# Kernel optimization log

Hardware: AMD Instinct MI355X
Metric: run time of the kernel (lower is better)

Reference implementation:

```python
import jax, jax.numpy as jnp
import numpy as np

B, SE, HD, ED, N, T = 64, 512, 1024, 512, 10000, 20
EOS_ID = 1
NEG_BIG = -1e9    # stand-in for -MAX_VAL encoder pad mask
MASK_VAL = -1e7   # logits_mask scatter value (-10000000.0 in torch)
M = HD + ED


def setup_inputs() -> dict:
    key = jax.random.key(0)
    ks = jax.random.split(key, 16)
    s = 0.02
    enc = jax.random.normal(ks[0], (B, SE, HD), jnp.float32)
    hidden = jax.random.normal(ks[1], (1, B, HD), jnp.float32)
    cell = jax.random.normal(ks[2], (1, B, HD), jnp.float32)
    text_lengths = jax.random.randint(ks[3], (B,), SE // 2, SE + 1)
    encoder_mask = jnp.arange(SE)[None, :] < text_lengths[:, None]  # [B,SE] bool
    embedding = jax.random.normal(ks[4], (N, ED), jnp.float32) * s
    # LSTM (PyTorch gate order i,f,g,o)
    w_ih = jax.random.normal(ks[5], (4 * HD, ED), jnp.float32) * s
    w_hh = jax.random.normal(ks[6], (4 * HD, HD), jnp.float32) * s
    b_ih = jnp.zeros((4 * HD,), jnp.float32)
    b_hh = jnp.zeros((4 * HD,), jnp.float32)
    # dense_net: Hd -> He
    w_q = jax.random.normal(ks[7], (HD, HD), jnp.float32) * s
    b_q = jnp.zeros((HD,), jnp.float32)
    # SelfAttentiveSum: Linear(Ed,Ed)+ReLU+Linear(Ed,1)
    w_k = jax.random.normal(ks[8], (ED, ED), jnp.float32) * s
    b_k = jnp.zeros((ED,), jnp.float32)
    w_ko = jax.random.normal(ks[9], (ED,), jnp.float32) * s
    b_ko = jnp.zeros((), jnp.float32)
    # MLP: Linear(M,M)+ReLU+Linear(M,N)
    w_m1 = jax.random.normal(ks[10], (M, M), jnp.float32) * s
    b_m1 = jnp.zeros((M,), jnp.float32)
    w_m2 = jax.random.normal(ks[11], (N, M), jnp.float32) * s
    b_m2 = jnp.zeros((N,), jnp.float32)
    return dict(encoded_hidden_embeddings=enc, hidden=hidden, cell=cell,
                text_lengths=text_lengths, encoder_mask=encoder_mask,
                embedding=embedding, w_ih=w_ih, w_hh=w_hh, b_ih=b_ih, b_hh=b_hh,
                w_q=w_q, b_q=b_q, w_k=w_k, b_k=b_k, w_ko=w_ko, b_ko=b_ko,
                w_m1=w_m1, b_m1=b_m1, w_m2=w_m2, b_m2=b_m2)


def _decode(enc, h0, c0, encoder_mask, embedding, w_ih, w_hh, b_ih, b_hh,
            w_q, b_q, w_k, b_k, w_ko, b_ko, w_m1, b_m1, w_m2, b_m2):
    pad_mask = jnp.where(encoder_mask, 0.0, NEG_BIG).astype(enc.dtype)  # [B,SE]
    sent = enc[:, 0, :]  # [B,HD] sentence representation (dropout is identity in eval)

    def step(carry, t):
        h, c, inp, logits_mask, buf = carry
        # --- LSTM cell (single step) ---
        gates = inp @ w_ih.T + b_ih + h @ w_hh.T + b_hh  # [B,4HD]
        i, f, g, o = jnp.split(gates, 4, axis=-1)
        c = jax.nn.sigmoid(f) * c + jax.nn.sigmoid(i) * jnp.tanh(g)
        h = jax.nn.sigmoid(o) * jnp.tanh(c)
        # --- attention over encoder states ---
        q = h @ w_q.T + b_q                                   # [B,HD]
        score = jnp.einsum('bsh,bh->bs', enc, q) + pad_mask    # [B,SE]
        w = jax.nn.softmax(score, axis=1)
        attn_enc = jnp.einsum('bs,bsh->bh', w, enc)            # [B,HD]
        # --- self-attentive sum over previously predicted label embeddings ---
        valid = jnp.arange(T) < jnp.maximum(t, 1)              # step 0: zeros row 0 valid
        k = jax.nn.relu(buf @ w_k.T + b_k) @ w_ko + b_ko       # [B,T]
        k = jnp.where(valid[None, :], k, NEG_BIG)
        sw = jax.nn.softmax(k, axis=1)
        attn_last = jnp.einsum('bt,bte->be', sw, buf)          # [B,ED]
        # --- MLP ---
        m = jnp.concatenate([sent + attn_enc, inp + attn_last], axis=-1)  # [B,M]
        logits = jax.nn.relu(m @ w_m1.T + b_m1) @ w_m2.T + b_m2 + logits_mask  # [B,N]
        next_ids = jnp.argmax(logits, axis=-1)                 # [B]
        pred_emb = embedding[next_ids]                          # [B,ED]
        buf = buf.at[:, t].set(pred_emb)
        logits_mask = logits_mask.at[jnp.arange(B), next_ids].set(MASK_VAL)
        logits_mask = logits_mask.at[:, EOS_ID].set(0.0)
        return (h, c, pred_emb, logits_mask, buf), (logits, next_ids)

    init = (h0, c0,
            jnp.zeros((B, ED), enc.dtype),
            jnp.zeros((B, N), enc.dtype),
            jnp.zeros((B, T, ED), enc.dtype))
    _, (outs, ids) = jax.lax.scan(step, init, jnp.arange(T))
    return jnp.transpose(outs, (1, 0, 2)), jnp.transpose(ids, (1, 0))  # [B,T,N],[B,T]


def reference(encoded_hidden_embeddings, hidden, cell, text_lengths, encoder_mask,
              embedding, w_ih, w_hh, b_ih, b_hh, w_q, b_q, w_k, b_k, w_ko, b_ko,
              w_m1, b_m1, w_m2, b_m2):
    # De=1: [1,B,HD] -> [B,HD]
    return _decode(encoded_hidden_embeddings, hidden[0], cell[0], encoder_mask,
                   embedding, w_ih, w_hh, b_ih, b_hh, w_q, b_q, w_k, b_k,
                   w_ko, b_ko, w_m1, b_m1, w_m2, b_m2)
```

## Files before the change

### kernel.cpp

```cpp
#include <hip/hip_runtime.h>

#define B64 64
#define SE 512
#define HD 1024
#define ED 512
#define NV 10000
#define TT 20
#define MM 1536
#define MASK_VALF -10000000.0f

#define OFF_XA    0
#define OFF_XB    98304
#define OFF_CT    196608
#define OFF_QF    262144
#define OFF_FM    327680
#define OFF_FL    328704
#define OFF_FACC  329728
#define OFF_XT2   1378304
#define OFF_H1T   1476608
#define OFF_ARGV  1574912
#define OFF_ARGI  1654912
#define OFF_MASKT 1734912
#define OFF_BUF   2374912
#define OFF_BUFT  3030272
#define OFF_KVP   3685632
#define OFF_LP    3767552

__device__ __forceinline__ float sigmoidf_(float x) { return 1.f / (1.f + expf(-x)); }

__global__ __launch_bounds__(256) void k_init(const float* __restrict__ h0,
                                              const float* __restrict__ c0,
                                              float* __restrict__ ws) {
  int idx = blockIdx.x * 256 + threadIdx.x, stride = gridDim.x * 256;
  float* xa = ws + OFF_XA;
  float* cT = ws + OFF_CT;
  float* maskT = ws + OFF_MASKT;
  float* buf = ws + OFF_BUF;
  float* bufT = ws + OFF_BUFT;
  for (int i = idx; i < 512 * 64; i += stride) xa[i] = 0.f;
  for (int i = idx; i < NV * 64; i += stride) maskT[i] = 0.f;
  for (int i = idx; i < B64 * TT * ED; i += stride) { buf[i] = 0.f; bufT[i] = 0.f; }
  for (int i = idx; i < HD * 64; i += stride) {
    int u = i >> 6, b = i & 63;
    xa[512 * 64 + i] = h0[b * HD + u];
    cT[i] = c0[b * HD + u];
  }
}

__global__ __launch_bounds__(256) void k_cell(const float* __restrict__ xcur,
                                              const float* __restrict__ w_ih,
                                              const float* __restrict__ w_hh,
                                              const float* __restrict__ b_ih,
                                              const float* __restrict__ b_hh,
                                              float* __restrict__ cT,
                                              float* __restrict__ xnext) {
  __shared__ float wl[8 * 1536];
  int tid = threadIdx.x;
  int u0 = blockIdx.x * 2;
  for (int i = tid; i < 3072; i += 256) {
    int lr = i / 384, kq = i % 384;
    int k = kq * 4;
    int grow = (lr >> 1) * 1024 + u0 + (lr & 1);
    float4 v;
    if (k < 512) v = *(const float4*)&w_ih[(size_t)grow * 512 + k];
    else v = *(const float4*)&w_hh[(size_t)grow * 1024 + (k - 512)];
    *(float4*)&wl[lr * 1536 + k] = v;
  }
  __syncthreads();
  int lane = tid & 63, wid = tid >> 6;
  int kbase = wid * 384;
  const float* xp = xcur + (size_t)kbase * 64 + lane;
  float acc[8] = {0, 0, 0, 0, 0, 0, 0, 0};
#pragma unroll 2
  for (int k4 = 0; k4 < 96; ++k4) {
    float x0 = xp[(4 * k4 + 0) * 64];
    float x1 = xp[(4 * k4 + 1) * 64];
    float x2 = xp[(4 * k4 + 2) * 64];
    float x3 = xp[(4 * k4 + 3) * 64];
#pragma unroll
    for (int lr = 0; lr < 8; ++lr) {
      const float4 w4 = *(const float4*)&wl[lr * 1536 + kbase + 4 * k4];
      acc[lr] = fmaf(w4.x, x0, acc[lr]);
      acc[lr] = fmaf(w4.y, x1, acc[lr]);
      acc[lr] = fmaf(w4.z, x2, acc[lr]);
      acc[lr] = fmaf(w4.w, x3, acc[lr]);
    }
  }
  __syncthreads();
#pragma unroll
  for (int lr = 0; lr < 8; ++lr) wl[wid * 512 + lr * 64 + lane] = acc[lr];
  __syncthreads();
  if (tid < 128) {
    int j = tid >> 6, b = tid & 63;
    float g4[4];
#pragma unroll
    for (int g = 0; g < 4; ++g) {
      int lr = g * 2 + j;
      int grow = g * 1024 + u0 + j;
      float v = b_ih[grow] + b_hh[grow];
#pragma unroll
      for (int w = 0; w < 4; ++w) v += wl[w * 512 + lr * 64 + b];
      g4[g] = v;
    }
    int u = u0 + j;
    float c = cT[u * 64 + b];
    float cn = sigmoidf_(g4[1]) * c + sigmoidf_(g4[0]) * tanhf(g4[2]);
    float hn = sigmoidf_(g4[3]) * tanhf(cn);
    cT[u * 64 + b] = cn;
    xnext[(512 + u) * 64 + b] = hn;
  }
}

__global__ __launch_bounds__(256) void k_q2(const float* __restrict__ h,
                                            const float* __restrict__ w_q,
                                            const float* __restrict__ b_q,
                                            float* __restrict__ qf) {
  __shared__ float wl[8 * 1024];
  int tid = threadIdx.x;
  int h0 = blockIdx.x * 8;
  for (int i = tid; i < 2048; i += 256) {
    int lr = i >> 8, kq = i & 255;
    *(float4*)&wl[lr * 1024 + kq * 4] = *(const float4*)&w_q[(size_t)(h0 + lr) * 1024 + kq * 4];
  }
  __syncthreads();
  int lane = tid & 63, wid = tid >> 6;
  int kbase = wid * 256;
  const float* xp = h + (size_t)kbase * 64 + lane;
  float acc[8] = {0, 0, 0, 0, 0, 0, 0, 0};
#pragma unroll 2
  for (int k4 = 0; k4 < 64; ++k4) {
    float x0 = xp[(4 * k4 + 0) * 64];
    float x1 = xp[(4 * k4 + 1) * 64];
    float x2 = xp[(4 * k4 + 2) * 64];
    float x3 = xp[(4 * k4 + 3) * 64];
#pragma unroll
    for (int lr = 0; lr < 8; ++lr) {
      const float4 w4 = *(const float4*)&wl[lr * 1024 + kbase + 4 * k4];
      acc[lr] = fmaf(w4.x, x0, acc[lr]);
      acc[lr] = fmaf(w4.y, x1, acc[lr]);
      acc[lr] = fmaf(w4.z, x2, acc[lr]);
      acc[lr] = fmaf(w4.w, x3, acc[lr]);
    }
  }
  __syncthreads();
#pragma unroll
  for (int lr = 0; lr < 8; ++lr) wl[wid * 512 + lr * 64 + lane] = acc[lr];
  __syncthreads();
  for (int e = tid; e < 512; e += 256) {
    int lr = e >> 6, b = e & 63;
    float v = b_q[h0 + lr];
#pragma unroll
    for (int w = 0; w < 4; ++w) v += wl[w * 512 + lr * 64 + b];
    qf[(size_t)b * 1024 + h0 + lr] = v;
  }
}

__global__ __launch_bounds__(256) void k_flash(const float* __restrict__ enc,
                                               const int* __restrict__ tlen,
                                               const float* __restrict__ qf,
                                               float* __restrict__ fm, float* __restrict__ fl,
                                               float* __restrict__ facc) {
  __shared__ float lacc[4][1024];
  __shared__ float lml[4][2];
  int b = blockIdx.x >> 4, split = blockIdx.x & 15;
  int tid = threadIdx.x, lane = tid & 63, wid = tid >> 6;
  int len = tlen[b];
  float qv[16];
#pragma unroll
  for (int j = 0; j < 4; ++j) {
    float4 tq = *(const float4*)&qf[(size_t)b * 1024 + j * 256 + lane * 4];
    qv[4 * j + 0] = tq.x; qv[4 * j + 1] = tq.y; qv[4 * j + 2] = tq.z; qv[4 * j + 3] = tq.w;
  }
  const float* base = enc + (size_t)b * SE * HD;
  int s0 = split * 32 + wid * 8;
  int nr = len - s0;
  nr = nr < 0 ? 0 : (nr > 8 ? 8 : nr);
  int npair = nr >> 1;

  float4 cA[4], cB[4], nA[4], nB[4];
  float m = -1e30f, l = 0.f, acc[16];
#pragma unroll
  for (int j = 0; j < 16; ++j) acc[j] = 0.f;

#define LOADROW(d, s)                                                 \
  {                                                                   \
    const float4* rp = (const float4*)(base + (size_t)(s)*HD) + lane; \
    d[0] = rp[0]; d[1] = rp[64]; d[2] = rp[128]; d[3] = rp[192];      \
  }

  if (npair > 0) { LOADROW(cA, s0); LOADROW(cB, s0 + 1); }
  for (int p = 0; p < npair; ++p) {
    if (p + 1 < npair) {
      LOADROW(nA, s0 + 2 * p + 2);
      LOADROW(nB, s0 + 2 * p + 3);
    } else if (nr & 1) {
      LOADROW(nA, s0 + nr - 1);
    }
    float d0 = 0.f, d1 = 0.f;
#pragma unroll
    for (int j = 0; j < 4; ++j) {
      d0 = fmaf(qv[4 * j + 0], cA[j].x, d0); d1 = fmaf(qv[4 * j + 0], cB[j].x, d1);
      d0 = fmaf(qv[4 * j + 1], cA[j].y, d0); d1 = fmaf(qv[4 * j + 1], cB[j].y, d1);
      d0 = fmaf(qv[4 * j + 2], cA[j].z, d0); d1 = fmaf(qv[4 * j + 2], cB[j].z, d1);
      d0 = fmaf(qv[4 * j + 3], cA[j].w, d0); d1 = fmaf(qv[4 * j + 3], cB[j].w, d1);
    }
#pragma unroll
    for (int off = 32; off; off >>= 1) { d0 += __shfl_xor(d0, off, 64); d1 += __shfl_xor(d1, off, 64); }
    d0 = __shfl(d0, 0, 64);
    d1 = __shfl(d1, 0, 64);
    float mn = fmaxf(m, fmaxf(d0, d1));
    float sc = expf(m - mn), p0 = expf(d0 - mn), p1 = expf(d1 - mn);
    l = l * sc + p0 + p1;
#pragma unroll
    for (int j = 0; j < 4; ++j) {
      acc[4 * j + 0] = fmaf(p1, cB[j].x, fmaf(p0, cA[j].x, acc[4 * j + 0] * sc));
      acc[4 * j + 1] = fmaf(p1, cB[j].y, fmaf(p0, cA[j].y, acc[4 * j + 1] * sc));
      acc[4 * j + 2] = fmaf(p1, cB[j].z, fmaf(p0, cA[j].z, acc[4 * j + 2] * sc));
      acc[4 * j + 3] = fmaf(p1, cB[j].w, fmaf(p0, cA[j].w, acc[4 * j + 3] * sc));
    }
    m = mn;
#pragma unroll
    for (int j = 0; j < 4; ++j) { cA[j] = nA[j]; cB[j] = nB[j]; }
  }
  if (nr & 1) {
    if (npair == 0) LOADROW(cA, s0);
    float d0 = 0.f;
#pragma unroll
    for (int j = 0; j < 4; ++j) {
      d0 = fmaf(qv[4 * j + 0], cA[j].x, d0);
      d0 = fmaf(qv[4 * j + 1], cA[j].y, d0);
      d0 = fmaf(qv[4 * j + 2], cA[j].z, d0);
      d0 = fmaf(qv[4 * j + 3], cA[j].w, d0);
    }
#pragma unroll
    for (int off = 32; off; off >>= 1) d0 += __shfl_xor(d0, off, 64);
    d0 = __shfl(d0, 0, 64);
    float mn = fmaxf(m, d0);
    float sc = expf(m - mn), p0 = expf(d0 - mn);
    l = l * sc + p0;
#pragma unroll
    for (int j = 0; j < 4; ++j) {
      acc[4 * j + 0] = fmaf(p0, cA[j].x, acc[4 * j + 0] * sc);
      acc[4 * j + 1] = fmaf(p0, cA[j].y, acc[4 * j + 1] * sc);
      acc[4 * j + 2] = fmaf(p0, cA[j].z, acc[4 * j + 2] * sc);
      acc[4 * j + 3] = fmaf(p0, cA[j].w, acc[4 * j + 3] * sc);
    }
    m = mn;
  }
#undef LOADROW
#pragma unroll
  for (int j = 0; j < 4; ++j)
    *(float4*)&lacc[wid][j * 256 + lane * 4] =
        make_float4(acc[4 * j], acc[4 * j + 1], acc[4 * j + 2], acc[4 * j + 3]);
  if (lane == 0) { lml[wid][0] = m; lml[wid][1] = l; }
  __syncthreads();
  float M = fmaxf(fmaxf(lml[0][0], lml[1][0]), fmaxf(lml[2][0], lml[3][0]));
  float w0 = expf(lml[0][0] - M), w1 = expf(lml[1][0] - M);
  float w2 = expf(lml[2][0] - M), w3 = expf(lml[3][0] - M);
  float L = w0 * lml[0][1] + w1 * lml[1][1] + w2 * lml[2][1] + w3 * lml[3][1];
  int p = b * 16 + split;
  for (int h = tid; h < 1024; h += 256)
    facc[(size_t)p * 1024 + h] =
        w0 * lacc[0][h] + w1 * lacc[1][h] + w2 * lacc[2][h] + w3 * lacc[3][h];
  if (tid == 0) { fm[p] = M; fl[p] = L; }
}

__global__ __launch_bounds__(256) void k_ctx(const float* __restrict__ enc,
                                             const float* __restrict__ fm,
                                             const float* __restrict__ fl,
                                             const float* __restrict__ facc,
                                             const float* __restrict__ kvp,
                                             const float* __restrict__ b_ko,
                                             const float* __restrict__ buf,
                                             const float* __restrict__ inpT,
                                             float* __restrict__ xT2, int tv) {
  __shared__ float pw[TT];
  int b = blockIdx.x >> 2, qd = blockIdx.x & 3;
  int tid = threadIdx.x;
  if (tid < tv) {
    float s = b_ko[0];
    for (int g = 0; g < 64; ++g) s += kvp[((size_t)g * TT + tid) * 64 + b];
    pw[tid] = s;
  }
  __syncthreads();
  float mx = -1e30f;
  for (int k = 0; k < tv; ++k) mx = fmaxf(mx, pw[k]);
  float den = 0.f;
  for (int k = 0; k < tv; ++k) den += expf(pw[k] - mx);
  float invd = 1.f / den;
  __syncthreads();
  if (tid < tv) pw[tid] = expf(pw[tid] - mx) * invd;
  __syncthreads();
  float M = -1e30f;
#pragma unroll
  for (int k = 0; k < 16; ++k) M = fmaxf(M, fm[b * 16 + k]);
  float w[16];
  float L = 0.f;
#pragma unroll
  for (int k = 0; k < 16; ++k) {
    w[k] = expf(fm[b * 16 + k] - M);
    L += w[k] * fl[b * 16 + k];
  }
  float inv = 1.f / L;
  {
    int h = qd * 256 + tid;
    float s = 0.f;
#pragma unroll
    for (int k = 0; k < 16; ++k) s += w[k] * facc[(size_t)(b * 16 + k) * 1024 + h];
    xT2[h * 64 + b] = enc[(size_t)b * SE * HD + h] + s * inv;
  }
  if (tid < 128) {
    int e = qd * 128 + tid;
    float a = 0.f;
    for (int k = 0; k < tv; ++k) a += pw[k] * buf[((size_t)b * TT + k) * 512 + e];
    xT2[(1024 + e) * 64 + b] = inpT[e * 64 + b] + a;
  }
}

__global__ __launch_bounds__(256) void k_h12(const float* __restrict__ xT2,
                                             const float* __restrict__ w_m1,
                                             const float* __restrict__ b_m1,
                                             float* __restrict__ h1T) {
  __shared__ float wl[8 * 1536];
  int tid = threadIdx.x;
  int r0 = blockIdx.x * 8;
  for (int i = tid; i < 3072; i += 256) {
    int lr = i / 384, kq = i % 384;
    *(float4*)&wl[lr * 1536 + kq * 4] = *(const float4*)&w_m1[(size_t)(r0 + lr) * MM + kq * 4];
  }
  __syncthreads();
  int lane = tid & 63, wid = tid >> 6;
  int kbase = wid * 384;
  const float* xp = xT2 + (size_t)kbase * 64 + lane;
  float acc[8] = {0, 0, 0, 0, 0, 0, 0, 0};
#pragma unroll 2
  for (int k4 = 0; k4 < 96; ++k4) {
    float x0 = xp[(4 * k4 + 0) * 64];
    float x1 = xp[(4 * k4 + 1) * 64];
    float x2 = xp[(4 * k4 + 2) * 64];
    float x3 = xp[(4 * k4 + 3) * 64];
#pragma unroll
    for (int lr = 0; lr < 8; ++lr) {
      const float4 w4 = *(const float4*)&wl[lr * 1536 + kbase + 4 * k4];
      acc[lr] = fmaf(w4.x, x0, acc[lr]);
      acc[lr] = fmaf(w4.y, x1, acc[lr]);
      acc[lr] = fmaf(w4.z, x2, acc[lr]);
      acc[lr] = fmaf(w4.w, x3, acc[lr]);
    }
  }
  __syncthreads();
#pragma unroll
  for (int lr = 0; lr < 8; ++lr) wl[wid * 512 + lr * 64 + lane] = acc[lr];
  __syncthreads();
  for (int e = tid; e < 512; e += 256) {
    int lr = e >> 6, b = e & 63;
    float v = b_m1[r0 + lr];
#pragma unroll
    for (int w = 0; w < 4; ++w) v += wl[w * 512 + lr * 64 + b];
    h1T[(size_t)(r0 + lr) * 64 + b] = fmaxf(v, 0.f);
  }
}

__global__ __launch_bounds__(256) void k_vocab(const float* __restrict__ h1T,
                                               const float* __restrict__ w_m2,
                                               float* __restrict__ lp) {
  __shared__ float Wl[128 * 36];
  __shared__ float Xl[32 * 68];
  int tid = threadIdx.x;
  int r0b = blockIdx.x * 128;
  int k0 = blockIdx.y * 256;
  int tc = tid & 15, tr = tid >> 4;
  int r0 = tr * 8, b0 = tc * 4;
  float4 acc[8];
#pragma unroll
  for (int i = 0; i < 8; ++i) acc[i] = make_float4(0.f, 0.f, 0.f, 0.f);
  for (int kt = 0; kt < 8; ++kt) {
    int kbase = k0 + kt * 32;
#pragma unroll
    for (int j = 0; j < 4; ++j) {
      int f = tid + 256 * j;
      int row = f >> 3, kkq = (f & 7) * 4;
      int gr = r0b + row;
      if (gr > NV - 1) gr = NV - 1;
      *(float4*)&Wl[row * 36 + kkq] = *(const float4*)&w_m2[(size_t)gr * MM + kbase + kkq];
    }
#pragma unroll
    for (int j = 0; j < 2; ++j) {
      int f = tid + 256 * j;
      int kk = f >> 4, bq = (f & 15) * 4;
      *(float4*)&Xl[kk * 68 + bq] = *(const float4*)&h1T[(size_t)(kbase + kk) * 64 + bq];
    }
    __syncthreads();
#pragma unroll 2
    for (int kq = 0; kq < 8; ++kq) {
      float4 xv0 = *(const float4*)&Xl[(kq * 4 + 0) * 68 + b0];
      float4 xv1 = *(const float4*)&Xl[(kq * 4 + 1) * 68 + b0];
      float4 xv2 = *(const float4*)&Xl[(kq * 4 + 2) * 68 + b0];
      float4 xv3 = *(const float4*)&Xl[(kq * 4 + 3) * 68 + b0];
#pragma unroll
      for (int i = 0; i < 8; ++i) {
        float4 av = *(const float4*)&Wl[(r0 + i) * 36 + kq * 4];
        acc[i].x = fmaf(av.x, xv0.x, acc[i].x);
        acc[i].y = fmaf(av.x, xv0.y, acc[i].y);
        acc[i].z = fmaf(av.x, xv0.z, acc[i].z);
        acc[i].w = fmaf(av.x, xv0.w, acc[i].w);
        acc[i].x = fmaf(av.y, xv1.x, acc[i].x);
        acc[i].y = fmaf(av.y, xv1.y, acc[i].y);
        acc[i].z = fmaf(av.y, xv1.z, acc[i].z);
        acc[i].w = fmaf(av.y, xv1.w, acc[i].w);
        acc[i].x = fmaf(av.z, xv2.x, acc[i].x);
        acc[i].y = fmaf(av.z, xv2.y, acc[i].y);
        acc[i].z = fmaf(av.z, xv2.z, acc[i].z);
        acc[i].w = fmaf(av.z, xv2.w, acc[i].w);
        acc[i].x = fmaf(av.w, xv3.x, acc[i].x);
        acc[i].y = fmaf(av.w, xv3.y, acc[i].y);
        acc[i].z = fmaf(av.w, xv3.z, acc[i].z);
        acc[i].w = fmaf(av.w, xv3.w, acc[i].w);
      }
    }
    __syncthreads();
  }
  float* o = lp + (size_t)blockIdx.y * 640000;
#pragma unroll
  for (int i = 0; i < 8; ++i) {
    int r = r0b + r0 + i;
    if (r < NV) *(float4*)&o[(size_t)r * 64 + b0] = acc[i];
  }
}

__global__ __launch_bounds__(256) void k_logfin(const float* __restrict__ lp,
                                                const float* __restrict__ b_m2,
                                                const float* __restrict__ maskT,
                                                float* __restrict__ argv, int* __restrict__ argi,
                                                float* __restrict__ out, int t) {
  __shared__ float tile[32][65];
  int lane = threadIdx.x & 63, wid = threadIdx.x >> 6;
  int rg = blockIdx.x * 4 + wid;
  int nb = blockIdx.x * 32;
  if (rg < 1250) {
    int r0 = rg * 8;
    float best = -3.4e38f;
    int bi = 0;
#pragma unroll
    for (int i = 0; i < 8; ++i) {
      int r = r0 + i;
      size_t idx = (size_t)r * 64 + lane;
      float v = b_m2[r] + maskT[idx];
#pragma unroll
      for (int s = 0; s < 6; ++s) v += lp[(size_t)s * 640000 + idx];
      tile[wid * 8 + i][lane] = v;
      if (v > best) { best = v; bi = r; }
    }
    argv[(size_t)rg * 64 + lane] = best;
    argi[(size_t)rg * 64 + lane] = bi;
  }
  __syncthreads();
  int b = threadIdx.x >> 2, q = threadIdx.x & 3;
  int nloc = q * 8;
  if (nb + nloc < NV) {
    float tmp[8];
#pragma unroll
    for (int c = 0; c < 8; ++c) tmp[c] = tile[nloc + c][b];
    float4* o = (float4*)&out[((size_t)b * TT + t) * NV + nb + nloc];
    o[0] = make_float4(tmp[0], tmp[1], tmp[2], tmp[3]);
    o[1] = make_float4(tmp[4], tmp[5], tmp[6], tmp[7]);
  }
}

__global__ __launch_bounds__(256) void k_final(const float* __restrict__ argv,
                                               const int* __restrict__ argi,
                                               const float* __restrict__ emb,
                                               float* __restrict__ maskT,
                                               float* __restrict__ xnext,
                                               float* __restrict__ buf, float* __restrict__ bufT,
                                               float* __restrict__ out_ids, int t) {
  __shared__ float sv[256];
  __shared__ int si_[256];
  __shared__ int sid;
  int b = blockIdx.x, tid = threadIdx.x;
  float best = -3.4e38f;
  int bi = 0x7fffffff;
  for (int g = tid; g < 1250; g += 256) {
    float v = argv[(size_t)g * 64 + b];
    int idx = argi[(size_t)g * 64 + b];
    if (v > best || (v == best && idx < bi)) { best = v; bi = idx; }
  }
  sv[tid] = best;
  si_[tid] = bi;
  __syncthreads();
  for (int off = 128; off; off >>= 1) {
    if (tid < off) {
      float v2 = sv[tid + off];
      int i2 = si_[tid + off];
      if (v2 > sv[tid] || (v2 == sv[tid] && i2 < si_[tid])) { sv[tid] = v2; si_[tid] = i2; }
    }
    __syncthreads();
  }
  if (tid == 0) {
    sid = si_[0];
    out_ids[b * TT + t] = (float)si_[0];
    if (si_[0] != 1) maskT[(size_t)si_[0] * 64 + b] = MASK_VALF;
  }
  __syncthreads();
  int id = sid;
  for (int e = tid; e < 512; e += 256) {
    float v = emb[(size_t)id * 512 + e];
    xnext[e * 64 + b] = v;
    buf[((size_t)b * TT + t) * 512 + e] = v;
    bufT[(size_t)e * (TT * 64) + t * 64 + b] = v;
  }
}

__global__ __launch_bounds__(256) void k_kscore(const float* __restrict__ bufT,
                                                const float* __restrict__ w_k,
                                                const float* __restrict__ b_k,
                                                const float* __restrict__ w_ko,
                                                float* __restrict__ kvp, int j) {
  __shared__ float sacc[4][8][64];
  int lane = threadIdx.x & 63, wid = threadIdx.x >> 6;
  int ug = blockIdx.x;
  int u0 = ug * 8;
  int k0 = wid * 128;
  const float* xp = bufT + (size_t)j * 64 + lane;
  float acc[8] = {0, 0, 0, 0, 0, 0, 0, 0};
  for (int k4 = 0; k4 < 32; ++k4) {
    int e = k0 + 4 * k4;
    float x0 = xp[(size_t)(e + 0) * (TT * 64)];
    float x1 = xp[(size_t)(e + 1) * (TT * 64)];
    float x2 = xp[(size_t)(e + 2) * (TT * 64)];
    float x3 = xp[(size_t)(e + 3) * (TT * 64)];
#pragma unroll
    for (int i = 0; i < 8; ++i) {
      const float4 w4 = *(const float4*)&w_k[(size_t)(u0 + i) * 512 + e];
      acc[i] = fmaf(w4.x, x0, acc[i]);
      acc[i] = fmaf(w4.y, x1, acc[i]);
      acc[i] = fmaf(w4.z, x2, acc[i]);
      acc[i] = fmaf(w4.w, x3, acc[i]);
    }
  }
#pragma unroll
  for (int i = 0; i < 8; ++i) sacc[wid][i][lane] = acc[i];
  __syncthreads();
  if (wid == 0) {
    float kp = 0.f;
#pragma unroll
    for (int i = 0; i < 8; ++i) {
      float tot = b_k[u0 + i] + sacc[0][i][lane] + sacc[1][i][lane] + sacc[2][i][lane] +
                  sacc[3][i][lane];
      kp += fmaxf(tot, 0.f) * w_ko[u0 + i];
    }
    kvp[((size_t)ug * TT + j) * 64 + lane] = kp;
  }
}

extern "C" void kernel_launch(void* const* d_in, const int* in_sizes, int n_in,
                              void* d_out, int out_size, void* d_ws, size_t ws_size,
                              hipStream_t stream) {
  const float* enc = (const float*)d_in[0];
  const float* h0 = (const float*)d_in[1];
  const float* c0 = (const float*)d_in[2];
  const int* tlen = (const int*)d_in[3];
  const float* emb = (const float*)d_in[5];
  const float* w_ih = (const float*)d_in[6];
  const float* w_hh = (const float*)d_in[7];
  const float* b_ih = (const float*)d_in[8];
  const float* b_hh = (const float*)d_in[9];
  const float* w_q = (const float*)d_in[10];
  const float* b_q = (const float*)d_in[11];
  const float* w_k = (const float*)d_in[12];
  const float* b_k = (const float*)d_in[13];
  const float* w_ko = (const float*)d_in[14];
  const float* b_ko = (const float*)d_in[15];
  const float* w_m1 = (const float*)d_in[16];
  const float* b_m1 = (const float*)d_in[17];
  const float* w_m2 = (const float*)d_in[18];
  const float* b_m2 = (const float*)d_in[19];

  float* ws = (float*)d_ws;
  float* out_logits = (float*)d_out;
  float* out_ids = out_logits + (size_t)B64 * TT * NV;

  k_init<<<2048, 256, 0, stream>>>(h0, c0, ws);
  k_kscore<<<64, 256, 0, stream>>>(ws + OFF_BUFT, w_k, b_k, w_ko, ws + OFF_KVP, 0);

  for (int t = 0; t < TT; ++t) {
    int tv = (t < 1) ? 1 : t;
    float* xcur = ws + ((t & 1) ? OFF_XB : OFF_XA);
    float* xnext = ws + ((t & 1) ? OFF_XA : OFF_XB);
    k_cell<<<512, 256, 0, stream>>>(xcur, w_ih, w_hh, b_ih, b_hh, ws + OFF_CT, xnext);
    k_q2<<<128, 256, 0, stream>>>(xnext + 512 * 64, w_q, b_q, ws + OFF_QF);
    k_flash<<<1024, 256, 0, stream>>>(enc, tlen, ws + OFF_QF, ws + OFF_FM, ws + OFF_FL,
                                      ws + OFF_FACC);
    k_ctx<<<256, 256, 0, stream>>>(enc, ws + OFF_FM, ws + OFF_FL, ws + OFF_FACC, ws + OFF_KVP,
                                   b_ko, ws + OFF_BUF, xcur, ws + OFF_XT2, tv);
    k_h12<<<192, 256, 0, stream>>>(ws + OFF_XT2, w_m1, b_m1, ws + OFF_H1T);
    k_vocab<<<dim3(79, 6), 256, 0, stream>>>(ws + OFF_H1T, w_m2, ws + OFF_LP);
    k_logfin<<<313, 256, 0, stream>>>(ws + OFF_LP, b_m2, ws + OFF_MASKT, ws + OFF_ARGV,
                                      (int*)(ws + OFF_ARGI), out_logits, t);
    k_final<<<64, 256, 0, stream>>>(ws + OFF_ARGV, (int*)(ws + OFF_ARGI), emb, ws + OFF_MASKT,
                                    xnext, ws + OFF_BUF, ws + OFF_BUFT, out_ids, t);
    if (t < TT - 1)
      k_kscore<<<64, 256, 0, stream>>>(ws + OFF_BUFT, w_k, b_k, w_ko, ws + OFF_KVP, t);
  }
}
```

Baseline: 3.178 ms.

## Halve vocab GEMM row tile and prefetch next K-slice into registers

The vocab projection kernel now handles 64 vocabulary rows per block instead of 128, which doubles the grid to 157x6 blocks so more of the GPU's compute units are busy. It also adds register double-buffering: the next 32-wide K slice of the weights and activations is loaded from global memory while the current slice is computed from LDS, then written to LDS after a barrier. This aims to hide global load latency and raise occupancy. The cost is that each activation tile is loaded once per 64 rows rather than per 128, and each thread does less work per LDS read.

```diff
diff --git a/kernel.cpp b/kernel.cpp
--- a/kernel.cpp
+++ b/kernel.cpp
@@ -364,41 +364,51 @@
 __global__ __launch_bounds__(256) void k_vocab(const float* __restrict__ h1T,
                                                const float* __restrict__ w_m2,
                                                float* __restrict__ lp) {
-  __shared__ float Wl[128 * 36];
+  __shared__ float Wl[64 * 36];
   __shared__ float Xl[32 * 68];
   int tid = threadIdx.x;
-  int r0b = blockIdx.x * 128;
+  int r0b = blockIdx.x * 64;
   int k0 = blockIdx.y * 256;
   int tc = tid & 15, tr = tid >> 4;
-  int r0 = tr * 8, b0 = tc * 4;
-  float4 acc[8];
-#pragma unroll
-  for (int i = 0; i < 8; ++i) acc[i] = make_float4(0.f, 0.f, 0.f, 0.f);
+  int r0 = tr * 4, b0 = tc * 4;
+  int wf1 = tid + 256;
+  int wrow0 = tid >> 3, wkq0 = (tid & 7) * 4;
+  int wrow1 = wf1 >> 3, wkq1 = (wf1 & 7) * 4;
+  int gr0 = r0b + wrow0; if (gr0 > NV - 1) gr0 = NV - 1;
+  int gr1 = r0b + wrow1; if (gr1 > NV - 1) gr1 = NV - 1;
+  int xk0 = tid >> 4, xb0 = (tid & 15) * 4;
+  int xk1 = wf1 >> 4, xb1 = (wf1 & 15) * 4;
+
+  float4 wp0 = *(const float4*)&w_m2[(size_t)gr0 * MM + k0 + wkq0];
+  float4 wp1 = *(const float4*)&w_m2[(size_t)gr1 * MM + k0 + wkq1];
+  float4 xp0 = *(const float4*)&h1T[(size_t)(k0 + xk0) * 64 + xb0];
+  float4 xp1 = *(const float4*)&h1T[(size_t)(k0 + xk1) * 64 + xb1];
+  *(float4*)&Wl[wrow0 * 36 + wkq0] = wp0;
+  *(float4*)&Wl[wrow1 * 36 + wkq1] = wp1;
+  *(float4*)&Xl[xk0 * 68 + xb0] = xp0;
+  *(float4*)&Xl[xk1 * 68 + xb1] = xp1;
+  __syncthreads();
+
+  float4 acc[4];
+#pragma unroll
+  for (int i = 0; i < 4; ++i) acc[i] = make_float4(0.f, 0.f, 0.f, 0.f);
+
   for (int kt = 0; kt < 8; ++kt) {
-    int kbase = k0 + kt * 32;
-#pragma unroll
-    for (int j = 0; j < 4; ++j) {
-      int f = tid + 256 * j;
-      int row = f >> 3, kkq = (f & 7) * 4;
-      int gr = r0b + row;
-      if (gr > NV - 1) gr = NV - 1;
-      *(float4*)&Wl[row * 36 + kkq] = *(const float4*)&w_m2[(size_t)gr * MM + kbase + kkq];
-    }
-#pragma unroll
-    for (int j = 0; j < 2; ++j) {
-      int f = tid + 256 * j;
-      int kk = f >> 4, bq = (f & 15) * 4;
-      *(float4*)&Xl[kk * 68 + bq] = *(const float4*)&h1T[(size_t)(kbase + kk) * 64 + bq];
-    }
-    __syncthreads();
-#pragma unroll 2
+    if (kt < 7) {
+      int kb = k0 + (kt + 1) * 32;
+      wp0 = *(const float4*)&w_m2[(size_t)gr0 * MM + kb + wkq0];
+      wp1 = *(const float4*)&w_m2[(size_t)gr1 * MM + kb + wkq1];
+      xp0 = *(const float4*)&h1T[(size_t)(kb + xk0) * 64 + xb0];
+      xp1 = *(const float4*)&h1T[(size_t)(kb + xk1) * 64 + xb1];
+    }
+#pragma unroll
     for (int kq = 0; kq < 8; ++kq) {
       float4 xv0 = *(const float4*)&Xl[(kq * 4 + 0) * 68 + b0];
       float4 xv1 = *(const float4*)&Xl[(kq * 4 + 1) * 68 + b0];
       float4 xv2 = *(const float4*)&Xl[(kq * 4 + 2) * 68 + b0];
       float4 xv3 = *(const float4*)&Xl[(kq * 4 + 3) * 68 + b0];
 #pragma unroll
-      for (int i = 0; i < 8; ++i) {
+      for (int i = 0; i < 4; ++i) {
         float4 av = *(const float4*)&Wl[(r0 + i) * 36 + kq * 4];
         acc[i].x = fmaf(av.x, xv0.x, acc[i].x);
         acc[i].y = fmaf(av.x, xv0.y, acc[i].y);
@@ -419,10 +429,17 @@
       }
     }
     __syncthreads();
+    if (kt < 7) {
+      *(float4*)&Wl[wrow0 * 36 + wkq0] = wp0;
+      *(float4*)&Wl[wrow1 * 36 + wkq1] = wp1;
+      *(float4*)&Xl[xk0 * 68 + xb0] = xp0;
+      *(float4*)&Xl[xk1 * 68 + xb1] = xp1;
+      __syncthreads();
+    }
   }
   float* o = lp + (size_t)blockIdx.y * 640000;
 #pragma unroll
-  for (int i = 0; i < 8; ++i) {
+  for (int i = 0; i < 4; ++i) {
     int r = r0b + r0 + i;
     if (r < NV) *(float4*)&o[(size_t)r * 64 + b0] = acc[i];
   }
@@ -594,7 +611,7 @@
     k_ctx<<<256, 256, 0, stream>>>(enc, ws + OFF_FM, ws + OFF_FL, ws + OFF_FACC, ws + OFF_KVP,
                                    b_ko, ws + OFF_BUF, xcur, ws + OFF_XT2, tv);
     k_h12<<<192, 256, 0, stream>>>(ws + OFF_XT2, w_m1, b_m1, ws + OFF_H1T);
-    k_vocab<<<dim3(79, 6), 256, 0, stream>>>(ws + OFF_H1T, w_m2, ws + OFF_LP);
+    k_vocab<<<dim3(157, 6), 256, 0, stream>>>(ws + OFF_H1T, w_m2, ws + OFF_LP);
     k_logfin<<<313, 256, 0, stream>>>(ws + OFF_LP, b_m2, ws + OFF_MASKT, ws + OFF_ARGV,
                                       (int*)(ws + OFF_ARGI), out_logits, t);
     k_final<<<64, 256, 0, stream>>>(ws + OFF_ARGV, (int*)(ws + OFF_ARGI), emb, ws + OFF_MASKT,
```

After: 3.444 ms. 8.4% more time.
